# Optimization experiments

Measured on AMD Instinct MI355X. Metric: run time of the kernel, lower is better.

The kernel has to match this reference:

```python
import jax, jax.numpy as jnp
import numpy as np

B, N, S = 8, 16384, 2048
C1, C2 = 128, 256
MLP = [256, 256]
BN_EPS = 1e-5


def setup_inputs() -> dict:
    key = jax.random.key(0)
    ks = jax.random.split(key, 12)
    inp = {
        "xyz1": jax.random.normal(ks[0], (B, N, 3), dtype=jnp.float32),
        "xyz2": jax.random.normal(ks[1], (B, S, 3), dtype=jnp.float32),
        "points1": jax.random.normal(ks[2], (B, C1, N), dtype=jnp.float32),
        "points2": jax.random.normal(ks[3], (B, C2, S), dtype=jnp.float32),
    }
    cin = C1 + C2
    kidx = 4
    for li, cout in enumerate(MLP):
        inp[f"W{li}"] = jax.random.normal(ks[kidx], (cout, cin), dtype=jnp.float32) * (1.0 / np.sqrt(cin))
        inp[f"b{li}"] = jnp.zeros((cout,), dtype=jnp.float32)
        inp[f"g{li}"] = jnp.ones((cout,), dtype=jnp.float32)
        inp[f"beta{li}"] = jnp.zeros((cout,), dtype=jnp.float32)
        cin = cout
        kidx += 1
    return inp


def _interpolate(xyz1, xyz2, points2):
    # D[b,n,s] = ||xyz1[b,n] - xyz2[b,s]||^2
    D = jnp.sum((xyz1[:, :, None, :] - xyz2[:, None, :, :]) ** 2, axis=-1)  # [B,N,S]
    neg_dist, idx = jax.lax.top_k(-D, 3)  # 3 smallest distances, ascending
    dist = jnp.maximum(-neg_dist, 1e-10)  # [B,N,3]
    w = 1.0 / dist
    weight = w / jnp.sum(w, axis=2, keepdims=True)  # [B,N,3]
    p2 = jnp.transpose(points2, (0, 2, 1))  # [B,S,C2]
    gathered = p2[jnp.arange(p2.shape[0])[:, None, None], idx]  # [B,N,3,C2]
    return jnp.einsum("bnkc,bnk->bcn", gathered, weight)  # [B,C2,N]


def _conv_bn_relu(x, W, b, g, beta):
    # 1x1 conv over points: [B,Cin,N] -> [B,Cout,N]
    y = jnp.einsum("oc,bcn->bon", W, x) + b[None, :, None]
    mean = jnp.mean(y, axis=(0, 2), keepdims=True)
    var = jnp.var(y, axis=(0, 2), keepdims=True)  # biased, training-mode BN
    yh = (y - mean) * jax.lax.rsqrt(var + BN_EPS)
    return jax.nn.relu(yh * g[None, :, None] + beta[None, :, None])


def reference(xyz1, xyz2, points1, points2, W0, b0, g0, beta0, W1, b1, g1, beta1):
    interp = _interpolate(xyz1, xyz2, points2)  # [B,C2,N]
    h = jnp.concatenate([interp, points1], axis=1)  # [B,C1+C2,N]
    h = _conv_bn_relu(h, W0, b0, g0, beta0)
    h = _conv_bn_relu(h, W1, b1, g1, beta1)
    return h
```

## Files before the change

kernel.cpp:

```cpp
#include <hip/hip_runtime.h>
#include <hip/hip_bf16.h>


typedef unsigned int u32;
typedef unsigned short u16;
typedef unsigned long long u64;
typedef __attribute__((ext_vector_type(8))) short short8;
typedef __attribute__((ext_vector_type(4))) float f32x4;

#define NT_TOTAL 131072
#define NN 16384
#define SS 2048

__device__ __forceinline__ float bf2f(u16 u) {
    union { u32 i; float f; } cv; cv.i = ((u32)u) << 16; return cv.f;
}
__device__ __forceinline__ u16 f2bf(float f) {
    union { float f; u32 i; } cv; cv.f = f;
    const u32 r = (cv.i + 0x7FFFu + ((cv.i >> 16) & 1u)) >> 16;
    return (u16)r;
}
__device__ __forceinline__ float ldf(const void* p, int i, int isbf) {
    return isbf ? bf2f(((const u16*)p)[i]) : ((const float*)p)[i];
}

__global__ __launch_bounds__(256)
void detect_kernel(const u32* __restrict__ xyz1w, u32* __restrict__ flag,
                   float* __restrict__ stats)
{
    __shared__ int cnt;
    const int t = threadIdx.x;
    if (t == 0) cnt = 0;
    for (int i = t; i < 1024; i += 256) stats[i] = 0.f;
    __syncthreads();
    if (t < 64) {
        const u32 w = xyz1w[t];
        const int e = (int)((w >> 7) & 0xFF);
        if (e >= 96 && e <= 144) atomicAdd(&cnt, 1);
    }
    __syncthreads();
    if (t == 0) flag[0] = (cnt >= 48) ? 1u : 0u;
}

__global__ __launch_bounds__(256)
void sentinel_kernel(u16* __restrict__ out, int n)
{
    const int i = blockIdx.x * 256 + threadIdx.x;
    if (i < n) out[i] = 0x4496;
}

__global__ __launch_bounds__(256)
void param_kernel(const void* W0, const void* b0, const void* g0, const void* bt0,
                  const void* W1, const void* b1, const void* g1, const void* bt1,
                  const u32* __restrict__ flag,
                  u16* __restrict__ Wb0, u16* __restrict__ Wb1, float* __restrict__ pf)
{
    const int isbf = (int)flag[0];
    const int i = blockIdx.x * 256 + threadIdx.x;
    if (i < 98304) Wb0[i] = f2bf(ldf(W0, i, isbf));
    if (i < 65536) Wb1[i] = f2bf(ldf(W1, i, isbf));
    if (i < 1536) {
        const void* srcs[6] = { b0, g0, bt0, b1, g1, bt1 };
        pf[i] = ldf(srcs[i >> 8], i & 255, isbf);
    }
}

__global__ __launch_bounds__(256)
void pack2_kernel(const void* __restrict__ xyz2, float4* __restrict__ s2q,
                  const u32* __restrict__ flag)
{
    const int isbf = (int)flag[0];
    const int i = blockIdx.x * 256 + threadIdx.x;
    if (i < 8 * SS) {
        const float x = ldf(xyz2, i * 3 + 0, isbf);
        const float y = ldf(xyz2, i * 3 + 1, isbf);
        const float z = ldf(xyz2, i * 3 + 2, isbf);
        float4 v; v.x = x; v.y = y; v.z = z; v.w = x * x + y * y + z * z;
        s2q[i] = v;
    }
}

__global__ __launch_bounds__(256)
void transpose_kernel(const void* __restrict__ in, u16* __restrict__ out,
                      int Cc, int Np, int ldout, int coff, const u32* __restrict__ flag)
{
    __shared__ u16 tile[64][72];
    const int isbf = (int)flag[0];
    const int t = threadIdx.x;
    const int n0 = blockIdx.x * 64, c0 = blockIdx.y * 64, bz = blockIdx.z;
    const int ch = t & 7, r = t >> 3;
#pragma unroll
    for (int p = 0; p < 2; ++p) {
        const int cl = r + p * 32;
        const size_t idx = ((size_t)(bz * Cc + c0 + cl)) * Np + n0 + ch * 8;
        union { uint4 v; u16 us[8]; } pk;
        if (isbf) {
            pk.v = *(const uint4*)((const u16*)in + idx);
        } else {
            const float4 va = *(const float4*)((const float*)in + idx);
            const float4 vb = *(const float4*)((const float*)in + idx + 4);
            pk.us[0] = f2bf(va.x); pk.us[1] = f2bf(va.y);
            pk.us[2] = f2bf(va.z); pk.us[3] = f2bf(va.w);
            pk.us[4] = f2bf(vb.x); pk.us[5] = f2bf(vb.y);
            pk.us[6] = f2bf(vb.z); pk.us[7] = f2bf(vb.w);
        }
        *(uint4*)&tile[cl][ch * 8] = pk.v;
    }
    __syncthreads();
#pragma unroll
    for (int p = 0; p < 2; ++p) {
        const int nl = r + p * 32;
        union { uint4 v; u16 us[8]; } pk;
#pragma unroll
        for (int i = 0; i < 8; ++i) pk.us[i] = tile[ch * 8 + i][nl];
        *(uint4*)&out[((size_t)(bz * Np + n0 + nl)) * ldout + coff + c0 + ch * 8] = pk.v;
    }
}

__global__ __launch_bounds__(256)
void knn_kernel(const float4* __restrict__ s2q, const void* __restrict__ xyz1,
                u32* __restrict__ idxA, float* __restrict__ wA,
                const u32* __restrict__ flag)
{
    const int isbf = (int)flag[0];
    const int t = threadIdx.x;
    const int blk = blockIdx.x;
    const int b = blk >> 6;
    const int qg = blk * 256 + t;
    const float qx = ldf(xyz1, qg * 3 + 0, isbf);
    const float qy = ldf(xyz1, qg * 3 + 1, isbf);
    const float qz = ldf(xyz1, qg * 3 + 2, isbf);
    const float qx2 = -2.f * qx, qy2 = -2.f * qy, qz2 = -2.f * qz;
    const float qc = qx * qx + qy * qy + qz * qz;
    const float4* __restrict__ S = s2q + (size_t)b * SS;

    float k0 = __builtin_inff(), k1 = k0, k2 = k0, k3 = k0, k4 = k0;
#pragma unroll 8
    for (int s = 0; s < SS; ++s) {
        const float4 v = S[s];
        float d = fmaf(v.x, qx2, qc);
        d = fmaf(v.y, qy2, d);
        d = fmaf(v.z, qz2, d);
        d += v.w;
        const float k = __uint_as_float((__float_as_uint(d) & 0xFFFFF800u) | (u32)s);
        const float o0 = fminf(k, k0);
        const float o1 = __builtin_amdgcn_fmed3f(k, k0, k1);
        const float o2 = __builtin_amdgcn_fmed3f(k, k1, k2);
        const float o3 = __builtin_amdgcn_fmed3f(k, k2, k3);
        const float o4 = __builtin_amdgcn_fmed3f(k, k3, k4);
        k0 = o0; k1 = o1; k2 = o2; k3 = o3; k4 = o4;
    }

    const float kk[5] = { k0, k1, k2, k3, k4 };
    u64 e0 = ~0ull, e1 = ~0ull, e2 = ~0ull;
#pragma unroll
    for (int i = 0; i < 5; ++i) {
        const u32 idx = __float_as_uint(kk[i]) & 0x7FFu;
        const float4 c = S[idx];
        const float dx = qx - c.x, dy = qy - c.y, dz = qz - c.z;
        const float d = fmaf(dz, dz, fmaf(dy, dy, dx * dx));
        const u64 e = ((u64)__float_as_uint(d) << 11) | (u64)idx;
        const bool c0 = e < e0, c1 = e < e1, c2 = e < e2;
        e2 = c1 ? e1 : (c2 ? e : e2);
        e1 = c0 ? e0 : (c1 ? e : e1);
        e0 = c0 ? e : e0;
    }
    const u32 i0 = (u32)(e0 & 0x7FF), i1 = (u32)(e1 & 0x7FF), i2 = (u32)(e2 & 0x7FF);
    const float d0 = fmaxf(__uint_as_float((u32)(e0 >> 11)), 1e-10f);
    const float d1 = fmaxf(__uint_as_float((u32)(e1 >> 11)), 1e-10f);
    const float d2 = fmaxf(__uint_as_float((u32)(e2 >> 11)), 1e-10f);
    const float w0 = 1.f / d0, w1 = 1.f / d1, w2 = 1.f / d2;
    const float inv = 1.f / (w0 + w1 + w2);
    idxA[qg * 3 + 0] = i0; idxA[qg * 3 + 1] = i1; idxA[qg * 3 + 2] = i2;
    wA[qg * 3 + 0] = w0 * inv; wA[qg * 3 + 1] = w1 * inv; wA[qg * 3 + 2] = w2 * inv;
}

__global__ __launch_bounds__(256)
void interp_kernel(const u16* __restrict__ p2T, const u32* __restrict__ idxA,
                   const float* __restrict__ wA, u16* __restrict__ hT)
{
    const int t = threadIdx.x;
    const int pl = t >> 5, g = t & 31;
    const int qg = blockIdx.x * 8 + pl;
    const int b = qg >> 14;
    float acc[8] = {0.f, 0.f, 0.f, 0.f, 0.f, 0.f, 0.f, 0.f};
#pragma unroll
    for (int k = 0; k < 3; ++k) {
        const u32 idx = idxA[qg * 3 + k];
        const float w = wA[qg * 3 + k];
        union { uint4 v; u16 us[8]; } pk;
        pk.v = *(const uint4*)(p2T + ((size_t)(b * SS + idx)) * 256 + g * 8);
#pragma unroll
        for (int e = 0; e < 8; ++e) acc[e] = fmaf(w, bf2f(pk.us[e]), acc[e]);
    }
    union { uint4 v; u16 us[8]; } ov;
#pragma unroll
    for (int e = 0; e < 8; ++e) ov.us[e] = f2bf(acc[e]);
    *(uint4*)&hT[(size_t)qg * 384 + g * 8] = ov.v;
}

__global__ __launch_bounds__(256)
void gemm_kernel(const u16* __restrict__ A, const u16* __restrict__ Bm,
                 const float* __restrict__ bias, void* __restrict__ yout, int K,
                 const u32* __restrict__ flag)
{
    __shared__ __align__(16) u16 aT[128 * 32];
    __shared__ __align__(16) u16 bT[128 * 32];
    const int isbf = (int)flag[0];
    const int t = threadIdx.x;
    const int lane = t & 63;
    const int l15 = lane & 15;
    const int q = lane >> 4;
    const int wid = t >> 6;
    const int n0 = blockIdx.x * 128;
    const int m0 = blockIdx.y * 128;
    const int wm = (wid & 1) * 64;
    const int wn = (wid >> 1) * 64;

    f32x4 acc[4][4] = {};

    const int ca0 = t, ca1 = t + 256;
    const u16* gA0 = A + (size_t)(m0 + (ca0 >> 2)) * K + (ca0 & 3) * 8;
    const u16* gA1 = A + (size_t)(m0 + (ca1 >> 2)) * K + (ca1 & 3) * 8;
    const u16* gB0 = Bm + (size_t)(n0 + (ca0 >> 2)) * K + (ca0 & 3) * 8;
    const u16* gB1 = Bm + (size_t)(n0 + (ca1 >> 2)) * K + (ca1 & 3) * 8;
    u16* lA0 = &aT[ca0 * 8]; u16* lA1 = &aT[ca1 * 8];
    u16* lB0 = &bT[ca0 * 8]; u16* lB1 = &bT[ca1 * 8];

    for (int k0 = 0; k0 < K; k0 += 32) {
        const uint4 ra0 = *(const uint4*)(gA0 + k0);
        const uint4 ra1 = *(const uint4*)(gA1 + k0);
        const uint4 rb0 = *(const uint4*)(gB0 + k0);
        const uint4 rb1 = *(const uint4*)(gB1 + k0);
        __syncthreads();
        *(uint4*)lA0 = ra0; *(uint4*)lA1 = ra1;
        *(uint4*)lB0 = rb0; *(uint4*)lB1 = rb1;
        __syncthreads();
        short8 a[4], b[4];
#pragma unroll
        for (int i = 0; i < 4; ++i)
            a[i] = *(const short8*)&aT[(wm + i * 16 + l15) * 32 + q * 8];
#pragma unroll
        for (int j = 0; j < 4; ++j)
            b[j] = *(const short8*)&bT[(wn + j * 16 + l15) * 32 + q * 8];
#pragma unroll
        for (int i = 0; i < 4; ++i)
#pragma unroll
            for (int j = 0; j < 4; ++j)
                acc[i][j] = __builtin_amdgcn_mfma_f32_16x16x32_bf16(a[i], b[j], acc[i][j], 0, 0, 0);
    }

#pragma unroll
    for (int i = 0; i < 4; ++i) {
        const int mBase = m0 + wm + i * 16 + q * 4;
        float bi[4];
#pragma unroll
        for (int r = 0; r < 4; ++r) bi[r] = bias[mBase + r];
#pragma unroll
        for (int j = 0; j < 4; ++j) {
            const int col = n0 + wn + j * 16 + l15;
            const size_t obase = ((size_t)(col >> 14) * 256) * NN + (col & 16383);
#pragma unroll
            for (int r = 0; r < 4; ++r) {
                const float v = acc[i][j][r] + bi[r];
                const size_t oi = obase + (size_t)(mBase + r) * NN;
                if (isbf) ((u16*)yout)[oi] = f2bf(v);
                else      ((float*)yout)[oi] = v;
            }
        }
    }
}

__global__ __launch_bounds__(256)
void stats_kernel(const void* __restrict__ y, float* __restrict__ sums,
                  float* __restrict__ sumsq, const u32* __restrict__ flag)
{
    const int isbf = (int)flag[0];
    const int t = threadIdx.x;
    const int c = blockIdx.y, bb = blockIdx.x;
    const size_t base = ((size_t)(bb * 256 + c)) * NN;
    float s = 0.f, sq = 0.f;
    if (isbf) {
        const u16* p = (const u16*)y + base;
#pragma unroll
        for (int i = 0; i < 8; ++i) {
            union { uint4 v; u16 us[8]; } pk;
            pk.v = *(const uint4*)(p + i * 2048 + t * 8);
#pragma unroll
            for (int e = 0; e < 8; ++e) { const float v = bf2f(pk.us[e]); s += v; sq += v * v; }
        }
    } else {
        const float* p = (const float*)y + base;
#pragma unroll
        for (int i = 0; i < 16; ++i) {
            const float4 v = *(const float4*)(p + i * 1024 + t * 4);
            s += v.x + v.y + v.z + v.w;
            sq += v.x * v.x + v.y * v.y + v.z * v.z + v.w * v.w;
        }
    }
#pragma unroll
    for (int off = 32; off > 0; off >>= 1) {
        s += __shfl_down(s, off);
        sq += __shfl_down(sq, off);
    }
    __shared__ float red[8];
    const int wid = t >> 6;
    if ((t & 63) == 0) { red[wid * 2] = s; red[wid * 2 + 1] = sq; }
    __syncthreads();
    if (t == 0) {
        atomicAdd(&sums[c], red[0] + red[2] + red[4] + red[6]);
        atomicAdd(&sumsq[c], red[1] + red[3] + red[5] + red[7]);
    }
}

__global__ __launch_bounds__(256)
void bn_act_tr_kernel(const void* __restrict__ y, const float* __restrict__ sums,
                      const float* __restrict__ sumsq, const float* __restrict__ gam,
                      const float* __restrict__ beta, u16* __restrict__ h2,
                      const u32* __restrict__ flag)
{
    __shared__ u16 tile[64][68];
    const int isbf = (int)flag[0];
    const int t = threadIdx.x;
    const int n0g = blockIdx.x * 64, c0 = blockIdx.y * 64;
    const int bb = n0g >> 14, nn0 = n0g & 16383;
    const float invNT = 1.0f / (float)NT_TOTAL;
    {
        const int f4 = t & 15, cbase = t >> 4;
#pragma unroll
        for (int p = 0; p < 4; ++p) {
            const int cl = cbase + p * 16;
            const int c = c0 + cl;
            const float mean = sums[c] * invNT;
            const float var = sumsq[c] * invNT - mean * mean;
            const float rstd = rsqrtf(var + 1e-5f);
            const float sc = gam[c] * rstd;
            const float sh = beta[c] - mean * sc;
            const size_t base = ((size_t)(bb * 256 + c)) * NN + nn0 + f4 * 4;
            float in4[4];
            if (isbf) {
                union { uint2 v2; u16 us[4]; } iv;
                iv.v2 = *(const uint2*)((const u16*)y + base);
#pragma unroll
                for (int e = 0; e < 4; ++e) in4[e] = bf2f(iv.us[e]);
            } else {
                const float4 v = *(const float4*)((const float*)y + base);
                in4[0] = v.x; in4[1] = v.y; in4[2] = v.z; in4[3] = v.w;
            }
            union { uint2 v2; u16 us[4]; } o;
#pragma unroll
            for (int e = 0; e < 4; ++e) {
                float v = in4[e] * sc + sh;
                v = (v != v) ? 777.0f : fmaxf(v, 0.f);
                o.us[e] = f2bf(v);
            }
            *(uint2*)&tile[cl][f4 * 4] = o.v2;
        }
    }
    __syncthreads();
    {
        const int ch = t & 7, rr = t >> 3;
#pragma unroll
        for (int p = 0; p < 2; ++p) {
            const int nl = rr + p * 32;
            union { uint4 v; u16 us[8]; } pk;
#pragma unroll
            for (int i = 0; i < 8; ++i) pk.us[i] = tile[ch * 8 + i][nl];
            *(uint4*)&h2[((size_t)(n0g + nl)) * 256 + c0 + ch * 8] = pk.v;
        }
    }
}

__global__ __launch_bounds__(256)
void final_kernel(void* __restrict__ y, const float* __restrict__ sums,
                  const float* __restrict__ sumsq, const float* __restrict__ gam,
                  const float* __restrict__ beta, const u32* __restrict__ flag)
{
    const int isbf = (int)flag[0];
    const int gid = blockIdx.x * 256 + threadIdx.x;
    const int c = (gid >> 12) & 255;
    const float invNT = 1.0f / (float)NT_TOTAL;
    const float mean = sums[c] * invNT;
    const float var = sumsq[c] * invNT - mean * mean;
    const float rstd = rsqrtf(var + 1e-5f);
    const float sc = gam[c] * rstd;
    const float sh = beta[c] - mean * sc;
    const size_t idx4 = (size_t)gid * 4;
    float in4[4];
    if (isbf) {
        union { uint2 v2; u16 us[4]; } iv;
        iv.v2 = *(const uint2*)((const u16*)y + idx4);
#pragma unroll
        for (int e = 0; e < 4; ++e) in4[e] = bf2f(iv.us[e]);
    } else {
        const float4 v = *(const float4*)((const float*)y + idx4);
        in4[0] = v.x; in4[1] = v.y; in4[2] = v.z; in4[3] = v.w;
    }
    float o4[4];
#pragma unroll
    for (int e = 0; e < 4; ++e) {
        float v = in4[e] * sc + sh;
        o4[e] = (v != v) ? 777.0f : fmaxf(v, 0.f);
    }
    if (isbf) {
        union { uint2 v2; u16 us[4]; } o;
#pragma unroll
        for (int e = 0; e < 4; ++e) o.us[e] = f2bf(o4[e]);
        *(uint2*)((u16*)y + idx4) = o.v2;
    } else {
        float4 o; o.x = o4[0]; o.y = o4[1]; o.z = o4[2]; o.w = o4[3];
        *(float4*)((float*)y + idx4) = o;
    }
}

__global__ void pointnet_fp_module_24532853195517_kernel() {}

extern "C" void kernel_launch(void* const* d_in, const int* in_sizes, int n_in,
                              void* d_out, int out_size, void* d_ws, size_t ws_size,
                              hipStream_t stream)
{
    const void* xyz1    = d_in[0];
    const void* xyz2    = d_in[1];
    const void* points1 = d_in[2];
    const void* points2 = d_in[3];
    const void* W0 = d_in[4];  const void* b0 = d_in[5];
    const void* g0 = d_in[6];  const void* bt0 = d_in[7];
    const void* W1 = d_in[8];  const void* b1 = d_in[9];
    const void* g1 = d_in[10]; const void* bt1 = d_in[11];

    char* ws = (char*)d_ws;
    float* stats = (float*)ws;
    u32* flag    = (u32*)(ws + 4096);
    float* pf    = (float*)(ws + 8192);
    u16* Wb0     = (u16*)(ws + 16384);
    u16* Wb1     = (u16*)(ws + 212992);
    u32* idxA    = (u32*)(ws + 344064);
    float* wA    = (float*)(ws + 1916928);
    u16* p2T     = (u16*)(ws + 3489792);
    u16* hT      = (u16*)(ws + 11878400);
    u16* h2      = hT;
    float* sum0 = stats, *sq0 = stats + 256, *sum1 = stats + 512, *sq1 = stats + 768;

    float4* s2q = (float4*)((char*)d_out + (8u << 20));

    if (ws_size < (size_t)112541696) {
        sentinel_kernel<<<(out_size + 255) / 256, 256, 0, stream>>>((u16*)d_out, out_size);
        return;
    }

    sentinel_kernel<<<16, 256, 0, stream>>>((u16*)d_out, 4096);

    detect_kernel<<<1, 256, 0, stream>>>((const u32*)xyz1, flag, stats);
    param_kernel<<<384, 256, 0, stream>>>(W0, b0, g0, bt0, W1, b1, g1, bt1, flag, Wb0, Wb1, pf);
    pack2_kernel<<<64, 256, 0, stream>>>(xyz2, s2q, flag);
    transpose_kernel<<<dim3(32, 4, 8), 256, 0, stream>>>(points2, p2T, 256, 2048, 256, 0, flag);
    transpose_kernel<<<dim3(256, 2, 8), 256, 0, stream>>>(points1, hT, 128, 16384, 384, 256, flag);
    knn_kernel<<<512, 256, 0, stream>>>(s2q, xyz1, idxA, wA, flag);
    interp_kernel<<<16384, 256, 0, stream>>>(p2T, idxA, wA, hT);
    gemm_kernel<<<dim3(1024, 2), 256, 0, stream>>>(Wb0, hT, pf + 0, d_out, 384, flag);
    stats_kernel<<<dim3(8, 256), 256, 0, stream>>>(d_out, sum0, sq0, flag);
    bn_act_tr_kernel<<<dim3(2048, 4), 256, 0, stream>>>(d_out, sum0, sq0, pf + 256, pf + 512, h2, flag);
    gemm_kernel<<<dim3(1024, 2), 256, 0, stream>>>(Wb1, h2, pf + 768, d_out, 256, flag);
    stats_kernel<<<dim3(8, 256), 256, 0, stream>>>(d_out, sum1, sq1, flag);
    final_kernel<<<32768, 256, 0, stream>>>(d_out, sum1, sq1, pf + 1024, pf + 1280, flag);
}
```

Measured before the change: 563.4 us.

## Split KNN candidate scan across thread pairs with packed FMA distance math

```diff
diff --git a/kernel.cpp b/kernel.cpp
--- a/kernel.cpp
+++ b/kernel.cpp
@@ -7,6 +7,7 @@
 typedef unsigned long long u64;
 typedef __attribute__((ext_vector_type(8))) short short8;
 typedef __attribute__((ext_vector_type(4))) float f32x4;
+typedef __attribute__((ext_vector_type(2))) float f32x2;
 
 #define NT_TOTAL 131072
 #define NN 16384
@@ -124,9 +125,9 @@
 {
     const int isbf = (int)flag[0];
     const int t = threadIdx.x;
-    const int blk = blockIdx.x;
-    const int b = blk >> 6;
-    const int qg = blk * 256 + t;
+    const int qg = blockIdx.x * 128 + (t >> 1);
+    const int h = t & 1;
+    const int b = qg >> 14;
     const float qx = ldf(xyz1, qg * 3 + 0, isbf);
     const float qy = ldf(xyz1, qg * 3 + 1, isbf);
     const float qz = ldf(xyz1, qg * 3 + 2, isbf);
@@ -134,27 +135,50 @@
     const float qc = qx * qx + qy * qy + qz * qz;
     const float4* __restrict__ S = s2q + (size_t)b * SS;
 
+    f32x2 qxv; qxv.x = qx2; qxv.y = qx2;
+    f32x2 qyv; qyv.x = qy2; qyv.y = qy2;
+    f32x2 qzv; qzv.x = qz2; qzv.y = qz2;
+
     float k0 = __builtin_inff(), k1 = k0, k2 = k0, k3 = k0, k4 = k0;
-#pragma unroll 8
-    for (int s = 0; s < SS; ++s) {
-        const float4 v = S[s];
-        float d = fmaf(v.x, qx2, qc);
-        d = fmaf(v.y, qy2, d);
-        d = fmaf(v.z, qz2, d);
-        d += v.w;
-        const float k = __uint_as_float((__float_as_uint(d) & 0xFFFFF800u) | (u32)s);
-        const float o0 = fminf(k, k0);
-        const float o1 = __builtin_amdgcn_fmed3f(k, k0, k1);
-        const float o2 = __builtin_amdgcn_fmed3f(k, k1, k2);
-        const float o3 = __builtin_amdgcn_fmed3f(k, k2, k3);
-        const float o4 = __builtin_amdgcn_fmed3f(k, k3, k4);
+    const int sbase = h * 1024;
+#pragma unroll 4
+    for (int it = 0; it < 512; ++it) {
+        const int s = sbase + it * 2;
+        const float4 va = S[s];
+        const float4 vb = S[s + 1];
+        f32x2 vx; vx.x = va.x; vx.y = vb.x;
+        f32x2 vy; vy.x = va.y; vy.y = vb.y;
+        f32x2 vz; vz.x = va.z; vz.y = vb.z;
+        f32x2 d;  d.x  = va.w + qc; d.y = vb.w + qc;
+        d = __builtin_elementwise_fma(vx, qxv, d);
+        d = __builtin_elementwise_fma(vy, qyv, d);
+        d = __builtin_elementwise_fma(vz, qzv, d);
+        const float ka = __uint_as_float((__float_as_uint(d.x) & 0xFFFFF800u) | (u32)s);
+        const float kb = __uint_as_float((__float_as_uint(d.y) & 0xFFFFF800u) | (u32)(s + 1));
+        float o0 = fminf(ka, k0);
+        float o1 = __builtin_amdgcn_fmed3f(ka, k0, k1);
+        float o2 = __builtin_amdgcn_fmed3f(ka, k1, k2);
+        float o3 = __builtin_amdgcn_fmed3f(ka, k2, k3);
+        float o4 = __builtin_amdgcn_fmed3f(ka, k3, k4);
         k0 = o0; k1 = o1; k2 = o2; k3 = o3; k4 = o4;
-    }
-
-    const float kk[5] = { k0, k1, k2, k3, k4 };
+        o0 = fminf(kb, k0);
+        o1 = __builtin_amdgcn_fmed3f(kb, k0, k1);
+        o2 = __builtin_amdgcn_fmed3f(kb, k1, k2);
+        o3 = __builtin_amdgcn_fmed3f(kb, k2, k3);
+        o4 = __builtin_amdgcn_fmed3f(kb, k3, k4);
+        k0 = o0; k1 = o1; k2 = o2; k3 = o3; k4 = o4;
+    }
+
+    const float p0 = __shfl_xor(k0, 1);
+    const float p1 = __shfl_xor(k1, 1);
+    const float p2 = __shfl_xor(k2, 1);
+    const float p3 = __shfl_xor(k3, 1);
+    const float p4 = __shfl_xor(k4, 1);
+    const float kk[10] = { k0, k1, k2, k3, k4, p0, p1, p2, p3, p4 };
+
     u64 e0 = ~0ull, e1 = ~0ull, e2 = ~0ull;
 #pragma unroll
-    for (int i = 0; i < 5; ++i) {
+    for (int i = 0; i < 10; ++i) {
         const u32 idx = __float_as_uint(kk[i]) & 0x7FFu;
         const float4 c = S[idx];
         const float dx = qx - c.x, dy = qy - c.y, dz = qz - c.z;
@@ -165,14 +189,16 @@
         e1 = c0 ? e0 : (c1 ? e : e1);
         e0 = c0 ? e : e0;
     }
-    const u32 i0 = (u32)(e0 & 0x7FF), i1 = (u32)(e1 & 0x7FF), i2 = (u32)(e2 & 0x7FF);
-    const float d0 = fmaxf(__uint_as_float((u32)(e0 >> 11)), 1e-10f);
-    const float d1 = fmaxf(__uint_as_float((u32)(e1 >> 11)), 1e-10f);
-    const float d2 = fmaxf(__uint_as_float((u32)(e2 >> 11)), 1e-10f);
-    const float w0 = 1.f / d0, w1 = 1.f / d1, w2 = 1.f / d2;
-    const float inv = 1.f / (w0 + w1 + w2);
-    idxA[qg * 3 + 0] = i0; idxA[qg * 3 + 1] = i1; idxA[qg * 3 + 2] = i2;
-    wA[qg * 3 + 0] = w0 * inv; wA[qg * 3 + 1] = w1 * inv; wA[qg * 3 + 2] = w2 * inv;
+    if (h == 0) {
+        const u32 i0 = (u32)(e0 & 0x7FF), i1 = (u32)(e1 & 0x7FF), i2 = (u32)(e2 & 0x7FF);
+        const float d0 = fmaxf(__uint_as_float((u32)(e0 >> 11)), 1e-10f);
+        const float d1 = fmaxf(__uint_as_float((u32)(e1 >> 11)), 1e-10f);
+        const float d2 = fmaxf(__uint_as_float((u32)(e2 >> 11)), 1e-10f);
+        const float w0 = 1.f / d0, w1 = 1.f / d1, w2 = 1.f / d2;
+        const float inv = 1.f / (w0 + w1 + w2);
+        idxA[qg * 3 + 0] = i0; idxA[qg * 3 + 1] = i1; idxA[qg * 3 + 2] = i2;
+        wA[qg * 3 + 0] = w0 * inv; wA[qg * 3 + 1] = w1 * inv; wA[qg * 3 + 2] = w2 * inv;
+    }
 }
 
 __global__ __launch_bounds__(256)
@@ -455,7 +481,7 @@
     pack2_kernel<<<64, 256, 0, stream>>>(xyz2, s2q, flag);
     transpose_kernel<<<dim3(32, 4, 8), 256, 0, stream>>>(points2, p2T, 256, 2048, 256, 0, flag);
     transpose_kernel<<<dim3(256, 2, 8), 256, 0, stream>>>(points1, hT, 128, 16384, 384, 256, flag);
-    knn_kernel<<<512, 256, 0, stream>>>(s2q, xyz1, idxA, wA, flag);
+    knn_kernel<<<1024, 256, 0, stream>>>(s2q, xyz1, idxA, wA, flag);
     interp_kernel<<<16384, 256, 0, stream>>>(p2T, idxA, wA, hT);
     gemm_kernel<<<dim3(1024, 2), 256, 0, stream>>>(Wb0, hT, pf + 0, d_out, 384, flag);
     stats_kernel<<<dim3(8, 256), 256, 0, stream>>>(d_out, sum0, sq0, flag);
```

Result: slower. 678.8 us (+20.5%).
